# Kernel tuning notes

Hardware: AMD Instinct MI355X
Metric: run time of the kernel (lower is better)

Reference implementation:

```python
import jax, jax.numpy as jnp
import numpy as np

WINDOW = (1, 5, 20)
FILL_VALUE = 1.0


def _boxsum(x, windows, dims):
    """Sliding-window sum with torch-style asymmetric 'same' padding (w//2, w - w//2 - 1)."""
    wd = [1] * x.ndim
    pads = [(0, 0)] * x.ndim
    for d, w in zip(dims, windows):
        wd[d] = w
        pads[d] = (w // 2, w - w // 2 - 1)
    return jax.lax.reduce_window(x, jnp.array(0, x.dtype), jax.lax.add,
                                 tuple(wd), (1,) * x.ndim, tuple(pads))


def setup_inputs() -> dict:
    key = jax.random.key(0)
    x = jax.random.normal(key, (256, 256, 1024), dtype=jnp.float32)
    return {"x": x}


def reference(x) -> jnp.ndarray:
    w0, w1, w2 = WINDOW
    # numerator: (sum over (w0, w1) window)^2, then summed over depth window w2
    num = _boxsum(x, (w0, w1), (0, 1)) ** 2
    num = _boxsum(num, (w2,), (2,))
    # denominator: sum of squares over full (w0, w1, w2) window
    denum = _boxsum(x * x, (w0, w1, w2), (0, 1, 2))
    # normalizing: count of valid elements in the (w0, w1) spatial window (conv2d of ones)
    norm = _boxsum(jnp.ones(x.shape[:2], dtype=x.dtype), (w0, w1), (0, 1))
    denum = denum * norm[:, :, None]
    return jnp.nan_to_num(num / denum, nan=FILL_VALUE)
```

## Files before the change

kernel.cpp:

```cpp
#include <hip/hip_runtime.h>
#include <math.h>

#define NI 256
#define NJ 256
#define NK 1024
#define JCHUNK 32
#define HALO 16
#define LROW (HALO + NK + HALO)

typedef float float4v __attribute__((ext_vector_type(4)));

__device__ __forceinline__ float finalize(float n, float d) {
    float r = n * __builtin_amdgcn_rcpf(d);
    if (!(r == r)) r = 1.0f;
    return r;
}

__device__ __forceinline__ void kwindow(const float* __restrict__ row, int base,
                                        float& w0, float& w1, float& w2, float& w3) {
    const float4v* p = (const float4v*)(row + HALO + base - 12);
    float4v q0 = p[0], q1 = p[1], q2 = p[2], q3 = p[3], q4 = p[4], q5 = p[5], q6 = p[6];
    float4v midv = (q1 + q2) + (q3 + q4);
    float mid = (midv[0] + midv[1]) + (midv[2] + midv[3]);
    w0 = q0[2] + q0[3] + mid + q5[0] + q5[1];
    w1 = w0 + q5[2] - q0[2];
    w2 = w1 + q5[3] - q0[3];
    w3 = w2 + q6[0] - q1[0];
}

__global__ __launch_bounds__(256)
void semblance_kernel(const float* __restrict__ x, float* __restrict__ out) {
    __shared__ __align__(16) float s_num[2][LROW];
    __shared__ __align__(16) float s_den[2][LROW];

    const int tid  = threadIdx.x;
    const int i    = blockIdx.y;
    const int j0   = blockIdx.x * JCHUNK;
    const int base = tid * 4;

    if (tid < HALO) {
        s_num[0][tid] = 0.f; s_den[0][tid] = 0.f;
        s_num[1][tid] = 0.f; s_den[1][tid] = 0.f;
        s_num[0][HALO + NK + tid] = 0.f; s_den[0][HALO + NK + tid] = 0.f;
        s_num[1][HALO + NK + tid] = 0.f; s_den[1][HALO + NK + tid] = 0.f;
    }

    const float* xk = x + (size_t)i * NJ * NK + base;

    float4v r0, r1, r2, r3, r4;
    r0 = (j0 - 2 >= 0) ? *(const float4v*)(xk + (size_t)(j0 - 2) * NK) : (float4v)0.f;
    r1 = (j0 - 1 >= 0) ? *(const float4v*)(xk + (size_t)(j0 - 1) * NK) : (float4v)0.f;
    r2 = *(const float4v*)(xk + (size_t)j0 * NK);
    r3 = (j0 + 1 < NJ) ? *(const float4v*)(xk + (size_t)(j0 + 1) * NK) : (float4v)0.f;
    r4 = (j0 + 2 < NJ) ? *(const float4v*)(xk + (size_t)(j0 + 2) * NK) : (float4v)0.f;
    float4v s = (r0 + r1) + (r2 + r3) + r4;
    float4v t = (r0 * r0 + r1 * r1) + (r2 * r2 + r3 * r3) + r4 * r4;

    #pragma unroll 2
    for (int jj = 0; jj < JCHUNK; ++jj) {
        const int j = j0 + jj;
        const int b = jj & 1;

        float4v un = s * s;
        *(float4v*)(&s_num[b][HALO + base]) = un;
        *(float4v*)(&s_den[b][HALO + base]) = t;

        float4v n = (float4v)0.f;
        if (j + 3 < NJ) n = *(const float4v*)(xk + (size_t)(j + 3) * NK);

        __syncthreads();

        float wn0, wn1, wn2, wn3, wd0, wd1, wd2, wd3;
        kwindow(s_num[b], base, wn0, wn1, wn2, wn3);
        kwindow(s_den[b], base, wd0, wd1, wd2, wd3);

        const int jlo = (j - 2 < 0) ? 0 : j - 2;
        const int jhi = (j + 2 > NJ - 1) ? NJ - 1 : j + 2;
        const float norm = (float)(jhi - jlo + 1);

        float4v o;
        o[0] = finalize(wn0, wd0 * norm);
        o[1] = finalize(wn1, wd1 * norm);
        o[2] = finalize(wn2, wd2 * norm);
        o[3] = finalize(wn3, wd3 * norm);
        __builtin_nontemporal_store(o, (float4v*)(out + ((size_t)i * NJ + j) * NK + base));

        s += n - r0;
        t += n * n - r0 * r0;
        r0 = r1; r1 = r2; r2 = r3; r3 = r4; r4 = n;
    }
}

extern "C" void kernel_launch(void* const* d_in, const int* in_sizes, int n_in,
                              void* d_out, int out_size, void* d_ws, size_t ws_size,
                              hipStream_t stream) {
    const float* x = (const float*)d_in[0];
    float* out = (float*)d_out;
    dim3 grid(NJ / JCHUNK, NI);
    semblance_kernel<<<grid, 256, 0, stream>>>(x, out);
}
```

Measured before the change: 96.53 us.

## Replace block-wide barrier with per-wave LDS segments and recomputed halos

```diff
diff --git a/kernel.cpp b/kernel.cpp
--- a/kernel.cpp
+++ b/kernel.cpp
@@ -5,8 +5,9 @@
 #define NJ 256
 #define NK 1024
 #define JCHUNK 32
-#define HALO 16
-#define LROW (HALO + NK + HALO)
+#define WPB 4
+#define KSEG 256
+#define WREG 288
 
 typedef float float4v __attribute__((ext_vector_type(4)));
 
@@ -16,9 +17,9 @@
     return r;
 }
 
-__device__ __forceinline__ void kwindow(const float* __restrict__ row, int base,
+__device__ __forceinline__ void kwindow(const float* __restrict__ p0,
                                         float& w0, float& w1, float& w2, float& w3) {
-    const float4v* p = (const float4v*)(row + HALO + base - 12);
+    const float4v* p = (const float4v*)p0;
     float4v q0 = p[0], q1 = p[1], q2 = p[2], q3 = p[3], q4 = p[4], q5 = p[5], q6 = p[6];
     float4v midv = (q1 + q2) + (q3 + q4);
     float mid = (midv[0] + midv[1]) + (midv[2] + midv[3]);
@@ -30,22 +31,32 @@
 
 __global__ __launch_bounds__(256)
 void semblance_kernel(const float* __restrict__ x, float* __restrict__ out) {
-    __shared__ __align__(16) float s_num[2][LROW];
-    __shared__ __align__(16) float s_den[2][LROW];
+    __shared__ __align__(16) float lds[WPB][2][WREG];
 
     const int tid  = threadIdx.x;
+    const int lane = tid & 63;
+    const int wave = tid >> 6;
     const int i    = blockIdx.y;
     const int j0   = blockIdx.x * JCHUNK;
-    const int base = tid * 4;
+    const int k0s  = wave * KSEG;
+    const int kb   = k0s + 4 * lane;
 
-    if (tid < HALO) {
-        s_num[0][tid] = 0.f; s_den[0][tid] = 0.f;
-        s_num[1][tid] = 0.f; s_den[1][tid] = 0.f;
-        s_num[0][HALO + NK + tid] = 0.f; s_den[0][HALO + NK + tid] = 0.f;
-        s_num[1][HALO + NK + tid] = 0.f; s_den[1][HALO + NK + tid] = 0.f;
+    float* Pn = &lds[wave][0][0];
+    float* Pd = &lds[wave][1][0];
+
+    const bool hal  = (lane < 6);
+    const int  hidx = (lane < 3) ? (4 + 4 * lane) : (272 + 4 * (lane - 3));
+    const int  hk   = k0s + hidx - 16;
+    const bool hok  = hal && (hk >= 0) && (hk < NK);
+
+    if (hal) {
+        *(float4v*)(Pn + hidx) = (float4v)0.f;
+        *(float4v*)(Pd + hidx) = (float4v)0.f;
     }
 
-    const float* xk = x + (size_t)i * NJ * NK + base;
+    const float* xi = x + (size_t)i * NJ * NK;
+    const float* xk = xi + kb;
+    const float* xh = xi + hk;
 
     float4v r0, r1, r2, r3, r4;
     r0 = (j0 - 2 >= 0) ? *(const float4v*)(xk + (size_t)(j0 - 2) * NK) : (float4v)0.f;
@@ -56,23 +67,42 @@
     float4v s = (r0 + r1) + (r2 + r3) + r4;
     float4v t = (r0 * r0 + r1 * r1) + (r2 * r2 + r3 * r3) + r4 * r4;
 
+    float4v hs = (float4v)0.f, ht = (float4v)0.f;
+    if (hok) {
+        #pragma unroll
+        for (int dj = -2; dj <= 2; ++dj) {
+            const int r = j0 + dj;
+            if (r >= 0 && r < NJ) {
+                float4v v = *(const float4v*)(xh + (size_t)r * NK);
+                hs += v; ht += v * v;
+            }
+        }
+    }
+
     #pragma unroll 2
     for (int jj = 0; jj < JCHUNK; ++jj) {
         const int j = j0 + jj;
-        const int b = jj & 1;
 
-        float4v un = s * s;
-        *(float4v*)(&s_num[b][HALO + base]) = un;
-        *(float4v*)(&s_den[b][HALO + base]) = t;
+        *(float4v*)(Pn + 16 + 4 * lane) = s * s;
+        *(float4v*)(Pd + 16 + 4 * lane) = t;
+        if (hok) {
+            *(float4v*)(Pn + hidx) = hs * hs;
+            *(float4v*)(Pd + hidx) = ht;
+        }
 
-        float4v n = (float4v)0.f;
+        float4v n = (float4v)0.f, hn = (float4v)0.f, hm = (float4v)0.f;
         if (j + 3 < NJ) n = *(const float4v*)(xk + (size_t)(j + 3) * NK);
+        if (hok) {
+            if (j + 3 < NJ) hn = *(const float4v*)(xh + (size_t)(j + 3) * NK);
+            if (j - 2 >= 0) hm = *(const float4v*)(xh + (size_t)(j - 2) * NK);
+        }
 
-        __syncthreads();
+        __builtin_amdgcn_wave_barrier();
+        asm volatile("" ::: "memory");
 
         float wn0, wn1, wn2, wn3, wd0, wd1, wd2, wd3;
-        kwindow(s_num[b], base, wn0, wn1, wn2, wn3);
-        kwindow(s_den[b], base, wd0, wd1, wd2, wd3);
+        kwindow(Pn + 4 + 4 * lane, wn0, wn1, wn2, wn3);
+        kwindow(Pd + 4 + 4 * lane, wd0, wd1, wd2, wd3);
 
         const int jlo = (j - 2 < 0) ? 0 : j - 2;
         const int jhi = (j + 2 > NJ - 1) ? NJ - 1 : j + 2;
@@ -83,11 +113,15 @@
         o[1] = finalize(wn1, wd1 * norm);
         o[2] = finalize(wn2, wd2 * norm);
         o[3] = finalize(wn3, wd3 * norm);
-        __builtin_nontemporal_store(o, (float4v*)(out + ((size_t)i * NJ + j) * NK + base));
+        __builtin_nontemporal_store(o, (float4v*)(out + ((size_t)i * NJ + j) * NK + kb));
 
         s += n - r0;
         t += n * n - r0 * r0;
         r0 = r1; r1 = r2; r2 = r3; r3 = r4; r4 = n;
+        if (hok) { hs += hn - hm; ht += hn * hn - hm * hm; }
+
+        __builtin_amdgcn_wave_barrier();
+        asm volatile("" ::: "memory");
     }
 }
 
```

Measured after the change: 92.68 us, median of 2. 1.04x faster.
